# Kernel optimization log

Hardware: AMD Instinct MI355X
Metric: run time of the kernel (lower is better)

Reference implementation:

```python
import jax, jax.numpy as jnp
import numpy as np

H = 1024
B_DIM = 64  # bottleneck
EPS = 1e-5

def setup_inputs() -> dict:
    key = jax.random.key(0)
    ks = jax.random.split(key, 5)
    x = jax.random.normal(ks[0], (8, 4096, H), dtype=jnp.float32)
    norm_w = jnp.ones((H,), jnp.float32)
    norm_b = jnp.zeros((H,), jnp.float32)
    # nn.Linear default init ~ U(-1/sqrt(fan_in), 1/sqrt(fan_in))
    lim_d = 1.0 / np.sqrt(H)
    down_w = jax.random.uniform(ks[1], (B_DIM, H), jnp.float32, -lim_d, lim_d)
    down_b = jax.random.uniform(ks[2], (B_DIM,), jnp.float32, -lim_d, lim_d)
    # NOTE: original inits up to zeros; we use small random values so the
    # computation (and gradients) are non-degenerate for kernel testing.
    lim_u = 1.0 / np.sqrt(B_DIM)
    up_w = jax.random.uniform(ks[3], (H, B_DIM), jnp.float32, -lim_u, lim_u)
    up_b = jax.random.uniform(ks[4], (H,), jnp.float32, -lim_u, lim_u)
    return {"x": x, "norm_w": norm_w, "norm_b": norm_b,
            "down_w": down_w, "down_b": down_b, "up_w": up_w, "up_b": up_b}

def reference(x, norm_w, norm_b, down_w, down_b, up_w, up_b):
    # LayerNorm over last dim, eps=1e-5 (PyTorch default)
    mu = jnp.mean(x, axis=-1, keepdims=True)
    var = jnp.mean(jnp.square(x - mu), axis=-1, keepdims=True)
    xn = (x - mu) * jax.lax.rsqrt(var + EPS) * norm_w + norm_b
    # down-proj [B,S,H] @ [H,b] -> [B,S,b]
    h = jnp.einsum('bsh,dh->bsd', xn, down_w) + down_b
    h = jax.nn.gelu(h, approximate=False)  # torch nn.GELU default = exact erf
    # up-proj [B,S,b] @ [b,H] -> [B,S,H], residual add
    out = jnp.einsum('bsd,hd->bsh', h, up_w) + up_b
    return x + out
```

## Files before the change

### kernel.cpp

```cpp
#include <hip/hip_runtime.h>


#define HDIM 1024
#define BDIM 64

using s16x8 = __attribute__((ext_vector_type(8))) short;
using s16x4 = __attribute__((ext_vector_type(4))) short;
using f32x4 = __attribute__((ext_vector_type(4))) float;

__device__ float g_wstat[128];

__device__ __forceinline__ short f2bf(float f) {
  unsigned u = __builtin_bit_cast(unsigned, f);
  u += 0x7fffu + ((u >> 16) & 1u);
  return (short)(u >> 16);
}
__device__ __forceinline__ float bf2f(short s) {
  unsigned u = ((unsigned)(unsigned short)s) << 16;
  return __builtin_bit_cast(float, u);
}

extern "C" __global__ void prep_weights(const float* __restrict__ dw,
                                        const float* __restrict__ uw,
                                        const float* __restrict__ nw,
                                        const float* __restrict__ nb,
                                        const float* __restrict__ db,
                                        short* __restrict__ wsbf) {
  const int b = blockIdx.x;
  if (b < 64) {
    int tid = b * 256 + threadIdx.x;
    if (tid < 8192) {
      int off = tid * 8;
      int k = off & (HDIM - 1);
      f32x4 v0 = *(const f32x4*)(dw + off);
      f32x4 v1 = *(const f32x4*)(dw + off + 4);
      f32x4 g0 = *(const f32x4*)(nw + k);
      f32x4 g1 = *(const f32x4*)(nw + k + 4);
      s16x8 o;
#pragma unroll
      for (int j = 0; j < 4; ++j) {
        o[j]     = f2bf(v0[j] * g0[j]);
        o[j + 4] = f2bf(v1[j] * g1[j]);
      }
      *(s16x8*)(wsbf + tid * 8) = o;
    } else {
      int off = (tid - 8192) * 8;
      f32x4 v0 = *(const f32x4*)(uw + off);
      f32x4 v1 = *(const f32x4*)(uw + off + 4);
      s16x8 o;
#pragma unroll
      for (int j = 0; j < 4; ++j) { o[j] = f2bf(v0[j]); o[j + 4] = f2bf(v1[j]); }
      *(s16x8*)(wsbf + tid * 8) = o;
    }
  } else {
    const int t = threadIdx.x;
    const int n = t >> 2, p = t & 3;
    const float* dwn = dw + n * HDIM;
    float s1 = 0.f, s2 = 0.f;
    for (int j = 0; j < 32; ++j) {
      int k = p * 256 + j * 8;
      f32x4 v0 = *(const f32x4*)(dwn + k);
      f32x4 v1 = *(const f32x4*)(dwn + k + 4);
      f32x4 g0 = *(const f32x4*)(nw + k);
      f32x4 g1 = *(const f32x4*)(nw + k + 4);
      f32x4 b0 = *(const f32x4*)(nb + k);
      f32x4 b1 = *(const f32x4*)(nb + k + 4);
#pragma unroll
      for (int jj = 0; jj < 4; ++jj) {
        s1 += bf2f(f2bf(v0[jj] * g0[jj])) + bf2f(f2bf(v1[jj] * g1[jj]));
        s2 += v0[jj] * b0[jj] + v1[jj] * b1[jj];
      }
    }
    s1 += __shfl_xor(s1, 1); s1 += __shfl_xor(s1, 2);
    s2 += __shfl_xor(s2, 1); s2 += __shfl_xor(s2, 2);
    if (p == 0) {
      g_wstat[n]      = s1;
      g_wstat[64 + n] = db[n] + s2;
    }
  }
}

extern "C" __global__ __launch_bounds__(256, 4)
void adapter_fused(const float* __restrict__ x,
                   const float* __restrict__ ub,
                   const short* __restrict__ dwb,
                   const short* __restrict__ uwb,
                   float* __restrict__ out)
{
  __shared__ __align__(16) short xbf[16 * 1024];
  __shared__ float muL[16];
  __shared__ float rsL[16];
  __shared__ __align__(16) short g[16][72];

  const int t    = threadIdx.x;
  const int w    = t >> 6;
  const int lane = t & 63;
  const int q    = lane >> 4;
  const int c    = lane & 15;
  const size_t rowbase = (size_t)blockIdx.x * 16;

  {
    const int r  = t >> 4;
    const int c2 = t & 15;
    const float* xrow = x + (rowbase + r) * HDIM;

    f32x4 v[16];
#pragma unroll
    for (int i = 0; i < 16; ++i) v[i] = ((const f32x4*)xrow)[i * 16 + c2];

    float sum = 0.f, ssq = 0.f;
#pragma unroll
    for (int i = 0; i < 16; ++i) {
      s16x4 o;
#pragma unroll
      for (int k = 0; k < 4; ++k) {
        float f = v[i][k]; sum += f; ssq += f * f; o[k] = f2bf(f);
      }
      int b = (i * 128 + c2 * 8) ^ ((r & 7) << 4);
      *(s16x4*)((char*)xbf + r * 2048 + b) = o;
    }
#pragma unroll
    for (int m = 1; m < 16; m <<= 1) {
      sum += __shfl_xor(sum, m);
      ssq += __shfl_xor(ssq, m);
    }
    if (c2 == 0) {
      float mu = sum * (1.0f / HDIM);
      muL[r] = mu;
      rsL[r] = rsqrtf(ssq * (1.0f / HDIM) - mu * mu + 1e-5f);
    }
  }
  __syncthreads();

  {
    const short* pB = dwb + (size_t)(w * 16 + c) * HDIM + q * 8;
    const char*  arow = (const char*)xbf + c * 2048;
    const int    sw   = (c & 7) << 4;
    f32x4 acc = {0.f, 0.f, 0.f, 0.f};
#pragma unroll 8
    for (int ks = 0; ks < 32; ++ks) {
      s16x8 a = *(const s16x8*)(arow + ((ks * 64 + q * 16) ^ sw));
      s16x8 b = *(const s16x8*)(pB + ks * 32);
      acc = __builtin_amdgcn_mfma_f32_16x16x32_bf16(a, b, acc, 0, 0, 0);
    }

    const float sdw = g_wstat[w * 16 + c];
    const float dbv = g_wstat[64 + w * 16 + c];
#pragma unroll
    for (int i = 0; i < 4; ++i) {
      const int m = q * 4 + i;
      float h = rsL[m] * (acc[i] - muL[m] * sdw) + dbv;
      g[m][w * 16 + c] = f2bf(0.5f * h * (1.0f + erff(h * 0.70710678118654752f)));
    }
  }
  __syncthreads();

  const s16x8 a0 = *(const s16x8*)&g[c][q * 8];
  const s16x8 a1 = *(const s16x8*)&g[c][32 + q * 8];

  const float* xr0 = x + (rowbase + q * 4 + 0) * HDIM + w * 256 + c;
  const float* xr1 = x + (rowbase + q * 4 + 1) * HDIM + w * 256 + c;
  const float* xr2 = x + (rowbase + q * 4 + 2) * HDIM + w * 256 + c;
  const float* xr3 = x + (rowbase + q * 4 + 3) * HDIM + w * 256 + c;
  float* or0 = out + (rowbase + q * 4 + 0) * HDIM + w * 256 + c;
  float* or1 = out + (rowbase + q * 4 + 1) * HDIM + w * 256 + c;
  float* or2 = out + (rowbase + q * 4 + 2) * HDIM + w * 256 + c;
  float* or3 = out + (rowbase + q * 4 + 3) * HDIM + w * 256 + c;
  const short* pu  = uwb + (size_t)(w * 256 + c) * BDIM + q * 8;
  const float* pub = ub + w * 256 + c;

#pragma unroll 4
  for (int nt = 0; nt < 16; ++nt) {
    const short* uwrow = pu + (size_t)nt * 16 * BDIM;
    s16x8 b0 = *(const s16x8*)(uwrow);
    s16x8 b1 = *(const s16x8*)(uwrow + 32);
    f32x4 o4 = {0.f, 0.f, 0.f, 0.f};
    o4 = __builtin_amdgcn_mfma_f32_16x16x32_bf16(a0, b0, o4, 0, 0, 0);
    o4 = __builtin_amdgcn_mfma_f32_16x16x32_bf16(a1, b1, o4, 0, 0, 0);
    const float ubv = pub[nt * 16];
    const int co = nt * 16;
    or0[co] = o4[0] + ubv + xr0[co];
    or1[co] = o4[1] + ubv + xr1[co];
    or2[co] = o4[2] + ubv + xr2[co];
    or3[co] = o4[3] + ubv + xr3[co];
  }
}

extern "C" void kernel_launch(void* const* d_in, const int* in_sizes, int n_in,
                              void* d_out, int out_size, void* d_ws, size_t ws_size,
                              hipStream_t stream) {
  const float* x  = (const float*)d_in[0];
  const float* nw = (const float*)d_in[1];
  const float* nb = (const float*)d_in[2];
  const float* dw = (const float*)d_in[3];
  const float* db = (const float*)d_in[4];
  const float* uw = (const float*)d_in[5];
  const float* ub = (const float*)d_in[6];
  float* out = (float*)d_out;

  short* wsbf = (short*)d_ws;
  prep_weights<<<65, 256, 0, stream>>>(dw, uw, nw, nb, db, wsbf);

  const int rows = in_sizes[0] / HDIM;
  const int grid = rows / 16;
  adapter_fused<<<grid, 256, 0, stream>>>(x, ub, wsbf, wsbf + 65536, out);
}
```

Measured before the change: 299.5 us.

## Stage fp32 x tile in LDS via direct global-to-LDS loads, reuse for residual

The 16-row x tile is now loaded into shared memory as fp32 with global_load_lds and padded rows, and the LayerNorm statistics and bf16 conversion are fused into the down-projection MFMA loop. The residual add reads x from LDS instead of re-reading it from global memory. The block grows to 512 threads with a split-K down-projection reduced through shared partials. This is meant to remove the second global read of x and overlap the loads, at the cost of about 64KB of LDS per block, which lowers occupancy.

```diff
diff --git a/kernel.cpp b/kernel.cpp
--- a/kernel.cpp
+++ b/kernel.cpp
@@ -1,11 +1,11 @@
 #include <hip/hip_runtime.h>
 
 
-#define HDIM 1024
-#define BDIM 64
+#define HDIM  1024
+#define BDIM  64
+#define XROWB 4112
 
 using s16x8 = __attribute__((ext_vector_type(8))) short;
-using s16x4 = __attribute__((ext_vector_type(4))) short;
 using f32x4 = __attribute__((ext_vector_type(4))) float;
 
 __device__ float g_wstat[128];
@@ -18,6 +18,13 @@
 __device__ __forceinline__ float bf2f(short s) {
   unsigned u = ((unsigned)(unsigned short)s) << 16;
   return __builtin_bit_cast(float, u);
+}
+
+__device__ __forceinline__ void gload16(const void* g, void* l) {
+  __builtin_amdgcn_global_load_lds(
+      (const __attribute__((address_space(1))) void*)g,
+      (__attribute__((address_space(3))) void*)l,
+      16, 0, 0);
 }
 
 extern "C" __global__ void prep_weights(const float* __restrict__ dw,
@@ -80,17 +87,18 @@
   }
 }
 
-extern "C" __global__ __launch_bounds__(256, 4)
+extern "C" __global__ __launch_bounds__(512, 4)
 void adapter_fused(const float* __restrict__ x,
                    const float* __restrict__ ub,
                    const short* __restrict__ dwb,
                    const short* __restrict__ uwb,
                    float* __restrict__ out)
 {
-  __shared__ __align__(16) short xbf[16 * 1024];
-  __shared__ float muL[16];
-  __shared__ float rsL[16];
+  __shared__ __align__(16) char  xf[16 * XROWB];
+  __shared__ __align__(16) float part[2][64][20];
   __shared__ __align__(16) short g[16][72];
+  __shared__ float shalf[2][16];
+  __shared__ float qhalf[2][16];
 
   const int t    = threadIdx.x;
   const int w    = t >> 6;
@@ -100,89 +108,85 @@
   const size_t rowbase = (size_t)blockIdx.x * 16;
 
   {
-    const int r  = t >> 4;
-    const int c2 = t & 15;
-    const float* xrow = x + (rowbase + r) * HDIM;
-
-    f32x4 v[16];
-#pragma unroll
-    for (int i = 0; i < 16; ++i) v[i] = ((const f32x4*)xrow)[i * 16 + c2];
-
+    const char* gx = (const char*)(x + rowbase * HDIM);
+#pragma unroll
+    for (int i = 0; i < 8; ++i) {
+      const int ch = w * 8 + i;
+      gload16(gx + ch * 1024 + lane * 16,
+              xf + (ch >> 2) * XROWB + (ch & 3) * 1024);
+    }
+  }
+  __syncthreads();
+
+  {
+    const int kh = w >> 2, nw = w & 3;
+    const char*  arow = xf + c * XROWB + kh * 2048;
+    const short* pB   = dwb + (size_t)(nw * 16 + c) * HDIM + kh * 512 + q * 8;
+    f32x4 acc = {0.f, 0.f, 0.f, 0.f};
     float sum = 0.f, ssq = 0.f;
 #pragma unroll
-    for (int i = 0; i < 16; ++i) {
-      s16x4 o;
-#pragma unroll
-      for (int k = 0; k < 4; ++k) {
-        float f = v[i][k]; sum += f; ssq += f * f; o[k] = f2bf(f);
-      }
-      int b = (i * 128 + c2 * 8) ^ ((r & 7) << 4);
-      *(s16x4*)((char*)xbf + r * 2048 + b) = o;
-    }
-#pragma unroll
-    for (int m = 1; m < 16; m <<= 1) {
-      sum += __shfl_xor(sum, m);
-      ssq += __shfl_xor(ssq, m);
-    }
-    if (c2 == 0) {
-      float mu = sum * (1.0f / HDIM);
-      muL[r] = mu;
-      rsL[r] = rsqrtf(ssq * (1.0f / HDIM) - mu * mu + 1e-5f);
-    }
+    for (int ks = 0; ks < 16; ++ks) {
+      f32x4 u0 = *(const f32x4*)(arow + ks * 128 + q * 32);
+      f32x4 u1 = *(const f32x4*)(arow + ks * 128 + q * 32 + 16);
+      s16x8 b = *(const s16x8*)(pB + ks * 32);
+      s16x8 a;
+#pragma unroll
+      for (int j = 0; j < 4; ++j) {
+        float f0 = u0[j]; sum += f0; ssq += f0 * f0; a[j]     = f2bf(f0);
+        float f1 = u1[j]; sum += f1; ssq += f1 * f1; a[j + 4] = f2bf(f1);
+      }
+      acc = __builtin_amdgcn_mfma_f32_16x16x32_bf16(a, b, acc, 0, 0, 0);
+    }
+    sum += __shfl_xor(sum, 16); sum += __shfl_xor(sum, 32);
+    ssq += __shfl_xor(ssq, 16); ssq += __shfl_xor(ssq, 32);
+    if (nw == 0 && lane < 16) { shalf[kh][c] = sum; qhalf[kh][c] = ssq; }
+    *(f32x4*)&part[kh][nw * 16 + c][q * 4] = acc;
   }
   __syncthreads();
 
+  if (w < 4) {
+    const int n = w * 16 + c;
+    f32x4 p0 = *(const f32x4*)&part[0][n][q * 4];
+    f32x4 p1 = *(const f32x4*)&part[1][n][q * 4];
+    f32x4 h4 = p0 + p1;
+    float sT = shalf[0][c] + shalf[1][c];
+    float qT = qhalf[0][c] + qhalf[1][c];
+    float muv = sT * (1.0f / HDIM);
+    float rsv = rsqrtf(qT * (1.0f / HDIM) - muv * muv + 1e-5f);
+    const float sdw = g_wstat[n];
+    const float dbv = g_wstat[64 + n];
+#pragma unroll
+    for (int i = 0; i < 4; ++i) {
+      const float m  = __shfl(muv, q * 4 + i);
+      const float rv = __shfl(rsv, q * 4 + i);
+      float h = rv * (h4[i] - m * sdw) + dbv;
+      g[q * 4 + i][n] = f2bf(0.5f * h * (1.0f + erff(h * 0.70710678118654752f)));
+    }
+  }
+  __syncthreads();
+
   {
-    const short* pB = dwb + (size_t)(w * 16 + c) * HDIM + q * 8;
-    const char*  arow = (const char*)xbf + c * 2048;
-    const int    sw   = (c & 7) << 4;
-    f32x4 acc = {0.f, 0.f, 0.f, 0.f};
-#pragma unroll 8
-    for (int ks = 0; ks < 32; ++ks) {
-      s16x8 a = *(const s16x8*)(arow + ((ks * 64 + q * 16) ^ sw));
-      s16x8 b = *(const s16x8*)(pB + ks * 32);
-      acc = __builtin_amdgcn_mfma_f32_16x16x32_bf16(a, b, acc, 0, 0, 0);
-    }
-
-    const float sdw = g_wstat[w * 16 + c];
-    const float dbv = g_wstat[64 + w * 16 + c];
-#pragma unroll
-    for (int i = 0; i < 4; ++i) {
-      const int m = q * 4 + i;
-      float h = rsL[m] * (acc[i] - muL[m] * sdw) + dbv;
-      g[m][w * 16 + c] = f2bf(0.5f * h * (1.0f + erff(h * 0.70710678118654752f)));
-    }
-  }
-  __syncthreads();
-
-  const s16x8 a0 = *(const s16x8*)&g[c][q * 8];
-  const s16x8 a1 = *(const s16x8*)&g[c][32 + q * 8];
-
-  const float* xr0 = x + (rowbase + q * 4 + 0) * HDIM + w * 256 + c;
-  const float* xr1 = x + (rowbase + q * 4 + 1) * HDIM + w * 256 + c;
-  const float* xr2 = x + (rowbase + q * 4 + 2) * HDIM + w * 256 + c;
-  const float* xr3 = x + (rowbase + q * 4 + 3) * HDIM + w * 256 + c;
-  float* or0 = out + (rowbase + q * 4 + 0) * HDIM + w * 256 + c;
-  float* or1 = out + (rowbase + q * 4 + 1) * HDIM + w * 256 + c;
-  float* or2 = out + (rowbase + q * 4 + 2) * HDIM + w * 256 + c;
-  float* or3 = out + (rowbase + q * 4 + 3) * HDIM + w * 256 + c;
-  const short* pu  = uwb + (size_t)(w * 256 + c) * BDIM + q * 8;
-  const float* pub = ub + w * 256 + c;
-
-#pragma unroll 4
-  for (int nt = 0; nt < 16; ++nt) {
-    const short* uwrow = pu + (size_t)nt * 16 * BDIM;
-    s16x8 b0 = *(const s16x8*)(uwrow);
-    s16x8 b1 = *(const s16x8*)(uwrow + 32);
-    f32x4 o4 = {0.f, 0.f, 0.f, 0.f};
-    o4 = __builtin_amdgcn_mfma_f32_16x16x32_bf16(a0, b0, o4, 0, 0, 0);
-    o4 = __builtin_amdgcn_mfma_f32_16x16x32_bf16(a1, b1, o4, 0, 0, 0);
-    const float ubv = pub[nt * 16];
-    const int co = nt * 16;
-    or0[co] = o4[0] + ubv + xr0[co];
-    or1[co] = o4[1] + ubv + xr1[co];
-    or2[co] = o4[2] + ubv + xr2[co];
-    or3[co] = o4[3] + ubv + xr3[co];
+    const s16x8 a0 = *(const s16x8*)&g[c][q * 8];
+    const s16x8 a1 = *(const s16x8*)&g[c][32 + q * 8];
+    const short* pu = uwb + (size_t)(w * 128 + c) * BDIM + q * 8;
+    float* ob = out + rowbase * HDIM + w * 128 + c;
+#pragma unroll 2
+    for (int nt = 0; nt < 8; ++nt) {
+      const short* uwrow = pu + (size_t)nt * 16 * BDIM;
+      s16x8 b0 = *(const s16x8*)(uwrow);
+      s16x8 b1 = *(const s16x8*)(uwrow + 32);
+      f32x4 o4 = {0.f, 0.f, 0.f, 0.f};
+      o4 = __builtin_amdgcn_mfma_f32_16x16x32_bf16(a0, b0, o4, 0, 0, 0);
+      o4 = __builtin_amdgcn_mfma_f32_16x16x32_bf16(a1, b1, o4, 0, 0, 0);
+      const int nc = w * 128 + nt * 16 + c;
+      const float ubv = ub[nc];
+#pragma unroll
+      for (int i = 0; i < 4; ++i) {
+        const int m = q * 4 + i;
+        float res = *(const float*)(xf + m * XROWB + nc * 4);
+        ob[(size_t)m * HDIM + nt * 16] = o4[i] + ubv + res;
+      }
+    }
   }
 }
 
@@ -203,5 +207,5 @@
 
   const int rows = in_sizes[0] / HDIM;
   const int grid = rows / 16;
-  adapter_fused<<<grid, 256, 0, stream>>>(x, ub, wsbf, wsbf + 65536, out);
-}
+  adapter_fused<<<grid, 512, 0, stream>>>(x, ub, wsbf, wsbf + 65536, out);
+}
```

Result: no change. 299.3 us (-0.1%).
